# Optimization experiments

Measured on AMD Instinct MI355X. Metric: run time of the kernel, lower is better.

## Reference

```python
import jax, jax.numpy as jnp
import numpy as np

B, D, F, P = 65536, 256, 512, 256


def setup_inputs() -> dict:
    key = jax.random.key(0)
    k_x, k_f, k_p, k_a, k_b, k_t = jax.random.split(key, 6)
    x = jax.random.normal(k_x, (B, D), dtype=jnp.float32)
    # reset_parameters: uniform(-0.27, 1)
    features = jax.random.uniform(k_f, (F, D), dtype=jnp.float32, minval=-0.27, maxval=1.0)
    prototypes = jax.random.uniform(k_p, (P, D), dtype=jnp.float32, minval=-0.27, maxval=1.0)
    # alpha/beta/theta init to zeros in the module; use small random values so the
    # output is non-trivial for kernel correctness checking.
    alpha = jax.random.normal(k_a, (1,), dtype=jnp.float32) * 0.1
    beta = jax.random.normal(k_b, (1,), dtype=jnp.float32) * 0.1
    theta = jax.random.normal(k_t, (1,), dtype=jnp.float32) * 0.1
    return {"x": x, "features": features, "prototypes": prototypes,
            "alpha": alpha, "beta": beta, "theta": theta}


def reference(x, features, prototypes, alpha, beta, theta):
    # Shared projections
    x_features = x @ features.T                 # [B, F]
    p_features = prototypes @ features.T        # [P, F]
    x_present = jax.nn.relu(x_features)         # [B, F]
    p_present = jax.nn.relu(p_features)         # [P, F]
    x_weighted = x_features * x_present         # [B, F]
    p_weighted = p_features * p_present         # [P, F]

    # Tversky terms
    common = x_weighted @ p_weighted.T                          # [B, P]
    x_weighted_sum = jnp.sum(x_weighted, axis=1, keepdims=True)  # [B, 1]
    x_p_interaction = x_weighted @ p_present.T                  # [B, P]
    x_distinctive = x_weighted_sum - x_p_interaction            # [B, P]
    p_weighted_sum = jnp.sum(p_weighted, axis=1)[None, :]        # [1, P]
    x_p_weighted_interaction = x_present @ p_weighted.T         # [B, P]
    p_distinctive = p_weighted_sum - x_p_weighted_interaction   # [B, P]

    return theta * common - alpha * x_distinctive - beta * p_distinctive
```

## Files before the change

### kernel.cpp

```cpp
#include <hip/hip_runtime.h>
#include <cstdint>
#include <cstddef>

#define Bsz 65536
#define Dsz 256
#define Fsz 512
#define Psz 256

typedef __attribute__((ext_vector_type(8))) short short8;
typedef __attribute__((ext_vector_type(4))) short short4v;
typedef __attribute__((ext_vector_type(4))) float float4v;
typedef __attribute__((ext_vector_type(16))) float float16v;
typedef __attribute__((ext_vector_type(4))) unsigned uint4v;

__device__ inline short f2bf(float f) {
    unsigned u = __builtin_bit_cast(unsigned, f);
    u = (u + 0x7FFFu + ((u >> 16) & 1u)) >> 16;
    return (short)u;
}
__device__ inline float bf2f(short s) {
    unsigned u = ((unsigned)(unsigned short)s) << 16;
    return __builtin_bit_cast(float, u);
}
__device__ inline unsigned cvt_pk_bf16(float lo, float hi) {
    unsigned r;
    asm("v_cvt_pk_bf16_f32 %0, %1, %2" : "=v"(r) : "v"(lo), "v"(hi));
    return r;
}
__device__ inline void gl_lds16(const short* g, short* lds) {
    __builtin_amdgcn_global_load_lds((const __attribute__((address_space(1))) unsigned*)g,
                                     (__attribute__((address_space(3))) unsigned*)lds,
                                     16, 0, 0);
}


#define SBPITCH 136

__global__ __launch_bounds__(256, 2) void k_pre(
    const float* __restrict__ prototypes, const float* __restrict__ features,
    const float* __restrict__ alpha_p, const float* __restrict__ beta_p,
    const float* __restrict__ theta_p,
    short* __restrict__ featbB, short* __restrict__ pab, float* __restrict__ pws_part)
{
    __shared__ char lds[65536 + 17408];
    short* FB = (short*)lds;
    short* As = (short*)(lds + 65536);
    short* Sb = (short*)(lds + 65536);

    const int t = threadIdx.x;
    const int w = t >> 6, lane = t & 63, l15 = lane & 15, l4 = lane >> 4;
    const int rowg = blockIdx.x >> 2, nc = blockIdx.x & 3;
    const float alpha = *alpha_p, beta = *beta_p, theta = *theta_p;

    #pragma unroll
    for (int it = 0; it < 16; ++it) {
        int u = it * 256 + t;
        int ftl = u >> 10, dtl = (u >> 6) & 15, ln = u & 63;
        const float* src = features + (size_t)(nc * 128 + ftl * 32 + (ln & 31)) * Dsz
                         + dtl * 16 + (ln >> 5) * 8;
        float4v v0 = *(const float4v*)src;
        float4v v1 = *(const float4v*)(src + 4);
        uint4v uv;
        uv.x = cvt_pk_bf16(v0.x, v0.y);
        uv.y = cvt_pk_bf16(v0.z, v0.w);
        uv.z = cvt_pk_bf16(v1.x, v1.y);
        uv.w = cvt_pk_bf16(v1.z, v1.w);
        short8 sv = __builtin_bit_cast(short8, uv);
        *(short8*)&FB[u * 8] = sv;
        if (rowg == 0) {
            int go = (((nc * 4 + ftl) * 16 + dtl) * 64 + ln) * 8;
            *(short8*)&featbB[go] = sv;
        }
    }

    float4v acc[2][4];
    #pragma unroll
    for (int a = 0; a < 2; ++a)
        #pragma unroll
        for (int b = 0; b < 4; ++b) acc[a][b] = (float4v){0.f, 0.f, 0.f, 0.f};

    const float* pbase = prototypes + (size_t)rowg * 64 * Dsz;

    for (int kc = 0; kc < 4; ++kc) {
        __syncthreads();
        #pragma unroll
        for (int j = 0; j < 4; ++j) {
            int idx = j * 1024 + t * 4;
            int r = idx >> 6, c = idx & 63;
            float4v v = *(const float4v*)(pbase + (size_t)r * Dsz + kc * 64 + c);
            int unit = r * 8 + ((c >> 3) ^ (r & 7));
            short4v s4; s4.x = f2bf(v.x); s4.y = f2bf(v.y); s4.z = f2bf(v.z); s4.w = f2bf(v.w);
            *(short4v*)((char*)As + unit * 16 + (c & 7) * 2) = s4;
        }
        __syncthreads();
        #pragma unroll
        for (int kk = 0; kk < 2; ++kk) {
            short8 af[2], bfr[4];
            const int k8 = kk * 4 + l4;
            #pragma unroll
            for (int tm = 0; tm < 2; ++tm) {
                int m = (w & 1) * 32 + tm * 16 + l15;
                af[tm] = *(const short8*)&As[(m * 8 + (k8 ^ (m & 7))) * 8];
            }
            #pragma unroll
            for (int tn = 0; tn < 4; ++tn) {
                int fl = ((w >> 1) * 4 + tn) * 16 + l15;
                int dtl = kc * 4 + kk * 2 + (l4 >> 1);
                int lnp = (fl & 31) + 32 * (l4 & 1);
                bfr[tn] = *(const short8*)&FB[(((fl >> 5) * 16 + dtl) * 64 + lnp) * 8];
            }
            #pragma unroll
            for (int tm = 0; tm < 2; ++tm)
                #pragma unroll
                for (int tn = 0; tn < 4; ++tn)
                    acc[tm][tn] = __builtin_amdgcn_mfma_f32_16x16x32_bf16(af[tm], bfr[tn], acc[tm][tn], 0, 0, 0);
        }
    }
    __syncthreads();
    #pragma unroll
    for (int tm = 0; tm < 2; ++tm)
        #pragma unroll
        for (int tn = 0; tn < 4; ++tn)
            #pragma unroll
            for (int r = 0; r < 4; ++r) {
                int row = (w & 1) * 32 + tm * 16 + l4 * 4 + r;
                int col = (w >> 1) * 64 + tn * 16 + l15;
                Sb[row * SBPITCH + col] = f2bf(acc[tm][tn][r]);
            }
    __syncthreads();
    #pragma unroll
    for (int rep = 0; rep < 4; ++rep) {
        int u = rep * 256 + t;
        int row = u >> 4, i = u & 15;
        short8 sv = *(const short8*)&Sb[row * SBPITCH + i * 8];
        uint4v u0, u1;
        float sum = 0.f;
        #pragma unroll
        for (int e = 0; e < 8; ++e) {
            float pf = bf2f(sv[e]);
            float pp = fmaxf(pf, 0.f);
            float pw = pf * pp;
            float a0 = theta * pw + alpha * (pp - 1.f);
            float b0 = beta * pw;
            sum += pw;
            unsigned pk = cvt_pk_bf16(a0, b0);
            if (e < 4) u0[e] = pk; else u1[e - 4] = pk;
        }
        int p = rowg * 64 + row;
        int c = 4 * nc + (i >> 2), s2 = i & 3, pt = p >> 5;
        int base = ((c * 4 + s2) * 8 + pt) * 512;
        *(short8*)&pab[base + (p & 31) * 8] = __builtin_bit_cast(short8, u0);
        *(short8*)&pab[base + ((p & 31) + 32) * 8] = __builtin_bit_cast(short8, u1);
        #pragma unroll
        for (int mk = 1; mk < 16; mk <<= 1) sum += __shfl_xor(sum, mk, 64);
        if (l15 == 0) pws_part[nc * 256 + p] = -beta * sum;
    }
}

__global__ __launch_bounds__(256, 2) void k_main(
    const float* __restrict__ x, const short* __restrict__ featbB,
    const short* __restrict__ pab, const float* __restrict__ pws_part,
    float* __restrict__ out)
{
    __shared__ short FBL[2][8192];
    __shared__ short PBL[16384];

    const int t = threadIdx.x;
    const int w = t >> 6, lane = t & 63, l31 = lane & 31, h = lane >> 5;
    const int mt = w & 1, pth = w >> 1;
    const size_t row0 = (size_t)blockIdx.x * 64;
    const int lane8 = lane * 8;

    auto stage_fb = [&](int cn, int buf) {
        const short* src = featbB + cn * 8192 + lane8;
        #pragma unroll
        for (int i = 0; i < 4; ++i)
            gl_lds16(src + (4 * w + i) * 512, &FBL[buf][(4 * w + i) * 512]);
    };
    auto stage_pab = [&](int cn) {
        const short* src = pab + (size_t)cn * 16384 + lane8;
        #pragma unroll
        for (int i = 0; i < 8; ++i)
            gl_lds16(src + (8 * w + i) * 512, &PBL[(8 * w + i) * 512]);
    };

    stage_fb(0, 0);
    stage_pab(0);
    __builtin_amdgcn_sched_barrier(0);

    short8 xf[16];
    {
        const float* xr = x + (row0 + mt * 32 + l31) * Dsz + h * 8;
        #pragma unroll
        for (int dt = 0; dt < 16; ++dt) {
            float4v v0 = *(const float4v*)(xr + dt * 16);
            float4v v1 = *(const float4v*)(xr + dt * 16 + 4);
            uint4v uv;
            uv.x = cvt_pk_bf16(v0.x, v0.y);
            uv.y = cvt_pk_bf16(v0.z, v0.w);
            uv.z = cvt_pk_bf16(v1.x, v1.y);
            uv.w = cvt_pk_bf16(v1.z, v1.w);
            xf[dt] = __builtin_bit_cast(short8, uv);
        }
    }

    float16v acc[4];
    #pragma unroll
    for (int a = 0; a < 4; ++a)
        #pragma unroll
        for (int e = 0; e < 16; ++e) acc[a][e] = 0.f;

    __syncthreads();

    #pragma unroll 1
    for (int c = 0; c < 16; ++c) {
        const int cur = c & 1;

        if (c) {
            __syncthreads();
            stage_pab(c);
        }
        if (c < 15) stage_fb(c + 1, cur ^ 1);
        __builtin_amdgcn_sched_barrier(0);

        float16v Ca, Cb;
        #pragma unroll
        for (int e = 0; e < 16; ++e) { Ca[e] = 0.f; Cb[e] = 0.f; }
        #pragma unroll
        for (int g = 0; g < 4; ++g) {
            short8 fbf[4];
            #pragma unroll
            for (int i = 0; i < 4; ++i)
                fbf[i] = *(const short8*)&FBL[cur][(g * 4 + i) * 512 + lane8];
            __builtin_amdgcn_s_setprio(1);
            #pragma unroll
            for (int i = 0; i < 4; ++i) {
                if (i & 1) Cb = __builtin_amdgcn_mfma_f32_32x32x16_bf16(fbf[i], xf[g * 4 + i], Cb, 0, 0, 0);
                else       Ca = __builtin_amdgcn_mfma_f32_32x32x16_bf16(fbf[i], xf[g * 4 + i], Ca, 0, 0, 0);
            }
            __builtin_amdgcn_s_setprio(0);
        }
        float16v C1;
        #pragma unroll
        for (int e = 0; e < 16; ++e) C1[e] = Ca[e] + Cb[e];

        __syncthreads();

        #pragma unroll
        for (int s = 0; s < 4; ++s) {
            short8 PBr[4];
            #pragma unroll
            for (int ptl = 0; ptl < 4; ++ptl)
                PBr[ptl] = *(const short8*)&PBL[(s * 8 + pth * 4 + ptl) * 512 + lane8];
            uint4v uf;
            #pragma unroll
            for (int q = 0; q < 4; ++q) {
                float xv = C1[4 * s + q];
                float xp = fmaxf(xv, 0.f);
                uf[q] = cvt_pk_bf16(xv * xp, xp);
            }
            short8 A2f = __builtin_bit_cast(short8, uf);
            __builtin_amdgcn_s_setprio(1);
            #pragma unroll
            for (int ptl = 0; ptl < 4; ++ptl)
                acc[ptl] = __builtin_amdgcn_mfma_f32_32x32x16_bf16(A2f, PBr[ptl], acc[ptl], 0, 0, 0);
            __builtin_amdgcn_s_setprio(0);
        }
    }

    #pragma unroll
    for (int ptl = 0; ptl < 4; ++ptl) {
        int pcol = (pth * 4 + ptl) * 32 + l31;
        float pn = pws_part[pcol] + pws_part[256 + pcol] + pws_part[512 + pcol] + pws_part[768 + pcol];
        #pragma unroll
        for (int r = 0; r < 16; ++r) {
            size_t m = row0 + mt * 32 + (r & 3) + 8 * (r >> 2) + 4 * h;
            out[m * Psz + pcol] = acc[ptl][r] + pn;
        }
    }
}

extern "C" void kernel_launch(void* const* d_in, const int* in_sizes, int n_in,
                              void* d_out, int out_size, void* d_ws, size_t ws_size,
                              hipStream_t stream) {
    const float* x          = (const float*)d_in[0];
    const float* features   = (const float*)d_in[1];
    const float* prototypes = (const float*)d_in[2];
    const float* alpha      = (const float*)d_in[3];
    const float* beta       = (const float*)d_in[4];
    const float* theta      = (const float*)d_in[5];
    float* out = (float*)d_out;

    char* ws = (char*)d_ws;
    short* featbB   = (short*)(ws);
    short* pab      = (short*)(ws + 262144);
    float* pws_part = (float*)(ws + 786432);

    hipLaunchKernelGGL(k_pre,  dim3(16),   dim3(256), 0, stream,
                       prototypes, features, alpha, beta, theta, featbB, pab, pws_part);
    hipLaunchKernelGGL(k_main, dim3(1024), dim3(256), 0, stream,
                       x, featbB, pab, pws_part, out);
}
```

Measured before the change: 188.8 us.

## Split stage-1 K reduction across wave pairs and load prototype fragments directly

Stage one (x·featuresᵀ) used to be computed redundantly by both pth wave pairs. It is now split along D, with each pair handling half the K dimension and exchanging partial sums through a small LDS buffer. This halves the first-stage MFMA work and the x registers needed per wave. Prototype B-fragments now load straight from global memory into registers instead of being staged in LDS, which frees LDS and drops one block-level staging step. The cost is an extra LDS exchange per chunk and global-load latency exposed inside the loop.

```diff
diff --git a/kernel.cpp b/kernel.cpp
--- a/kernel.cpp
+++ b/kernel.cpp
@@ -163,13 +163,15 @@
     float* __restrict__ out)
 {
     __shared__ short FBL[2][8192];
-    __shared__ short PBL[16384];
+    __shared__ float EXC[4096];
 
     const int t = threadIdx.x;
     const int w = t >> 6, lane = t & 63, l31 = lane & 31, h = lane >> 5;
     const int mt = w & 1, pth = w >> 1;
     const size_t row0 = (size_t)blockIdx.x * 64;
     const int lane8 = lane * 8;
+    const int excW = (mt * 2 + pth) * 1024 + lane * 4;
+    const int excR = (mt * 2 + (pth ^ 1)) * 1024 + lane * 4;
 
     auto stage_fb = [&](int cn, int buf) {
         const short* src = featbB + cn * 8192 + lane8;
@@ -177,30 +179,23 @@
         for (int i = 0; i < 4; ++i)
             gl_lds16(src + (4 * w + i) * 512, &FBL[buf][(4 * w + i) * 512]);
     };
-    auto stage_pab = [&](int cn) {
-        const short* src = pab + (size_t)cn * 16384 + lane8;
-        #pragma unroll
-        for (int i = 0; i < 8; ++i)
-            gl_lds16(src + (8 * w + i) * 512, &PBL[(8 * w + i) * 512]);
-    };
 
     stage_fb(0, 0);
-    stage_pab(0);
     __builtin_amdgcn_sched_barrier(0);
 
-    short8 xf[16];
+    short8 xf[8];
     {
-        const float* xr = x + (row0 + mt * 32 + l31) * Dsz + h * 8;
-        #pragma unroll
-        for (int dt = 0; dt < 16; ++dt) {
-            float4v v0 = *(const float4v*)(xr + dt * 16);
-            float4v v1 = *(const float4v*)(xr + dt * 16 + 4);
+        const float* xr = x + (row0 + mt * 32 + l31) * Dsz + pth * 128 + h * 8;
+        #pragma unroll
+        for (int i = 0; i < 8; ++i) {
+            float4v v0 = *(const float4v*)(xr + i * 16);
+            float4v v1 = *(const float4v*)(xr + i * 16 + 4);
             uint4v uv;
             uv.x = cvt_pk_bf16(v0.x, v0.y);
             uv.y = cvt_pk_bf16(v0.z, v0.w);
             uv.z = cvt_pk_bf16(v1.x, v1.y);
             uv.w = cvt_pk_bf16(v1.z, v1.w);
-            xf[dt] = __builtin_bit_cast(short8, uv);
+            xf[i] = __builtin_bit_cast(short8, uv);
         }
     }
 
@@ -216,10 +211,13 @@
     for (int c = 0; c < 16; ++c) {
         const int cur = c & 1;
 
-        if (c) {
-            __syncthreads();
-            stage_pab(c);
-        }
+        if (c) __syncthreads();
+
+        const short* pb = pab + (size_t)c * 16384 + lane8;
+        short8 PA[8];
+        #pragma unroll
+        for (int k = 0; k < 8; ++k)
+            PA[k] = *(const short8*)(pb + ((k >> 2) * 8 + pth * 4 + (k & 3)) * 512);
         if (c < 15) stage_fb(c + 1, cur ^ 1);
         __builtin_amdgcn_sched_barrier(0);
 
@@ -227,11 +225,11 @@
         #pragma unroll
         for (int e = 0; e < 16; ++e) { Ca[e] = 0.f; Cb[e] = 0.f; }
         #pragma unroll
-        for (int g = 0; g < 4; ++g) {
+        for (int g = 0; g < 2; ++g) {
             short8 fbf[4];
             #pragma unroll
             for (int i = 0; i < 4; ++i)
-                fbf[i] = *(const short8*)&FBL[cur][(g * 4 + i) * 512 + lane8];
+                fbf[i] = *(const short8*)&FBL[cur][(pth * 8 + g * 4 + i) * 512 + lane8];
             __builtin_amdgcn_s_setprio(1);
             #pragma unroll
             for (int i = 0; i < 4; ++i) {
@@ -240,18 +238,35 @@
             }
             __builtin_amdgcn_s_setprio(0);
         }
+        float16v Cp;
+        #pragma unroll
+        for (int e = 0; e < 16; ++e) Cp[e] = Ca[e] + Cb[e];
+
+        #pragma unroll
+        for (int q = 0; q < 4; ++q)
+            *(float4v*)&EXC[excW + q * 256] =
+                (float4v){Cp[4 * q], Cp[4 * q + 1], Cp[4 * q + 2], Cp[4 * q + 3]};
+
+        __syncthreads();
+
+        short8 PB2[8];
+        #pragma unroll
+        for (int k = 0; k < 8; ++k)
+            PB2[k] = *(const short8*)(pb + ((2 + (k >> 2)) * 8 + pth * 4 + (k & 3)) * 512);
+        __builtin_amdgcn_sched_barrier(0);
+
         float16v C1;
         #pragma unroll
-        for (int e = 0; e < 16; ++e) C1[e] = Ca[e] + Cb[e];
-
-        __syncthreads();
+        for (int q = 0; q < 4; ++q) {
+            float4v o = *(const float4v*)&EXC[excR + q * 256];
+            C1[4 * q]     = Cp[4 * q]     + o.x;
+            C1[4 * q + 1] = Cp[4 * q + 1] + o.y;
+            C1[4 * q + 2] = Cp[4 * q + 2] + o.z;
+            C1[4 * q + 3] = Cp[4 * q + 3] + o.w;
+        }
 
         #pragma unroll
         for (int s = 0; s < 4; ++s) {
-            short8 PBr[4];
-            #pragma unroll
-            for (int ptl = 0; ptl < 4; ++ptl)
-                PBr[ptl] = *(const short8*)&PBL[(s * 8 + pth * 4 + ptl) * 512 + lane8];
             uint4v uf;
             #pragma unroll
             for (int q = 0; q < 4; ++q) {
@@ -262,8 +277,10 @@
             short8 A2f = __builtin_bit_cast(short8, uf);
             __builtin_amdgcn_s_setprio(1);
             #pragma unroll
-            for (int ptl = 0; ptl < 4; ++ptl)
-                acc[ptl] = __builtin_amdgcn_mfma_f32_32x32x16_bf16(A2f, PBr[ptl], acc[ptl], 0, 0, 0);
+            for (int ptl = 0; ptl < 4; ++ptl) {
+                short8 pfrag = (s < 2) ? PA[s * 4 + ptl] : PB2[(s - 2) * 4 + ptl];
+                acc[ptl] = __builtin_amdgcn_mfma_f32_32x32x16_bf16(A2f, pfrag, acc[ptl], 0, 0, 0);
+            }
             __builtin_amdgcn_s_setprio(0);
         }
     }
```

Result: faster. 180.4 us (-4.5%).
